# Performance work log

Measured on AMD Instinct MI355X. Metric: run time of the kernel, lower is better.

## Reference

```python
import jax, jax.numpy as jnp
import numpy as np

# parameter limits (low, high) as in Filter_param.limits
LIMITS = {
    'f_start': (200.0, 4000.0),
    'f_inf': (20.0, 500.0),
    'f_decay': (0.0, 2.0),
    'f_T': (0.0, 2.0),
    'w_offset': (0.0, 1.0),
    'w_T': (0.01, 0.5),
}

B, T = 2048, 8192

def setup_inputs() -> dict:
    key = jax.random.key(0)
    ks = jax.random.split(key, 7)
    return {
        'X': jax.random.normal(ks[0], (B, T), dtype=jnp.float32),
        'F': 44100,  # sampling frequency (int constant)
        'f_start_normal': jax.random.normal(ks[1], (), dtype=jnp.float32),
        'f_inf_normal': jax.random.normal(ks[2], (), dtype=jnp.float32),
        'f_decay_normal': jax.random.normal(ks[3], (), dtype=jnp.float32),
        'f_T_normal': jax.random.normal(ks[4], (), dtype=jnp.float32),
        'w_offset_normal': jax.random.normal(ks[5], (), dtype=jnp.float32),
        'w_T_normal': jax.random.normal(ks[6], (), dtype=jnp.float32),
    }

def _squash(v, name):
    low, high = LIMITS[name]
    return low + (high - low) * jax.nn.sigmoid(v)

def reference(X, F, f_start_normal, f_inf_normal, f_decay_normal,
              f_T_normal, w_offset_normal, w_T_normal):
    Bsz, Tlen = X.shape
    c = (2.0 ** (1.0 / 3.0) - 1.0) ** 0.5 * F / np.pi  # scalar cutoff constant
    t = jnp.arange(Tlen, dtype=X.dtype) / Tlen  # normalized time [T]

    f_start = _squash(f_start_normal, 'f_start')
    f_inf = _squash(f_inf_normal, 'f_inf')
    f_decay = _squash(f_decay_normal, 'f_decay')
    f_T = _squash(f_T_normal, 'f_T')
    w_offset = _squash(w_offset_normal, 'w_offset')
    w_T = _squash(w_T_normal, 'w_T')

    # time-varying cutoff frequency and output window
    f = f_inf + (f_start - f_inf) * (0.7 * 0.1 ** f_decay) ** (t / (10.0 * 0.1 ** f_T))  # [T]
    w = jax.nn.sigmoid((t - w_offset) / w_T)  # [T]
    a = (f - c) / (f + c)  # [T]
    b = (a + 1.0) / 2.0    # [T]

    # cascaded time-varying one-pole recurrence (two stages), scanned over time.
    # t=0: y1 = y2 = X[:,0];   t>0:
    #   y1[t] = b[t]*(x[t] + x[t-1]) - a[t]*y1[t-1]
    #   y2[t] = b[t]*(y1[t] + y1[t-1]) - a[t]*y2[t-1]
    x0 = X[:, 0]
    init = (x0, x0, x0, w[0] * x0)  # (y0_prev, y1_prev, y2_prev, acc)

    def step(carry, inp):
        y0p, y1p, y2p, acc = carry
        x_t, a_t, b_t, w_t = inp
        y1 = b_t * (x_t + y0p) - a_t * y1p
        y2 = b_t * (y1 + y1p) - a_t * y2p
        return (x_t, y1, y2, acc + w_t * y2), None

    xs = (X[:, 1:].T, a[1:], b[1:], w[1:])  # time-major [T-1, ...]
    (_, _, _, acc), _ = jax.lax.scan(step, init, xs)

    return acc / jnp.sum(w)  # prediction [B]
```

## Files before the change

### kernel.cpp

```cpp
#include <hip/hip_runtime.h>
#include <math.h>

#define BB 2048
#define TT 8192
#define CC 128
#define LL 64

#define OFF_SC  2048
#define OFF_Q   4096

__device__ inline float sigmoid_dev(float v) { return 1.0f / (1.0f + expf(-v)); }
__device__ inline float squash_dev(float v, float lo, float hi) {
    return lo + (hi - lo) * sigmoid_dev(v);
}

struct SquashedParams {
    float c, f_start, f_inf, log2K_invTd, w_offset, inv_w_T;
};

__device__ inline SquashedParams load_params(const int* Fp,
                                             const float* p_fstart, const float* p_finf,
                                             const float* p_fdecay, const float* p_fT,
                                             const float* p_woff, const float* p_wT) {
    SquashedParams P;
    float Fv      = (float)(*Fp);
    P.c           = sqrtf(exp2f(1.0f / 3.0f) - 1.0f) * Fv / 3.14159265358979323846f;
    P.f_start     = squash_dev(*p_fstart, 200.0f, 4000.0f);
    P.f_inf       = squash_dev(*p_finf,   20.0f,  500.0f);
    float f_decay = squash_dev(*p_fdecay, 0.0f,   2.0f);
    float f_T     = squash_dev(*p_fT,     0.0f,   2.0f);
    P.w_offset    = squash_dev(*p_woff,   0.0f,   1.0f);
    float w_T     = squash_dev(*p_wT,     0.01f,  0.5f);
    P.inv_w_T     = 1.0f / w_T;
    const float LOG2_10 = 3.32192809488736235f;
    float log2K  = log2f(0.7f) - LOG2_10 * f_decay;
    float invTd  = 0.1f * exp2f(LOG2_10 * f_T);
    P.log2K_invTd = log2K * invTd;
    return P;
}

__device__ inline float4 step_coef(const SquashedParams& P, int tg) {
    if (tg >= TT - 1) return make_float4(0.0f, 0.0f, 0.0f, 0.0f);
    float ti = (float)(tg + 1) * (1.0f / (float)TT);
    float f  = P.f_inf + (P.f_start - P.f_inf) * exp2f(P.log2K_invTd * ti);
    float a  = (f - P.c) / (f + P.c);
    float b  = 0.5f * (a + 1.0f);
    float m  = -a;
    float p  = b * (1.0f + m);
    float w  = sigmoid_dev((ti - P.w_offset) * P.inv_w_T);
    return make_float4(m, b, p, w);
}

__global__ void setup_kernel(const int* Fp,
                             const float* p_fstart, const float* p_finf,
                             const float* p_fdecay, const float* p_fT,
                             const float* p_woff, const float* p_wT,
                             float4* __restrict__ A4, float* __restrict__ SC) {
    int j = threadIdx.x;
    SquashedParams P = load_params(Fp, p_fstart, p_finf, p_fdecay, p_fT, p_woff, p_wT);
    float al = 1.0f, be = 0.0f, ga = 0.0f, de = 0.0f, ws = 0.0f;
    for (int k = 0; k < LL; k++) {
        float4 c4 = step_coef(P, j * LL + k);
        float m = c4.x, p = c4.z, w = c4.w;
        float nal = m * al;
        float nbe = fmaf(p, al, m * be);
        de = fmaf(w * m, al, de);
        ga = fmaf(w, nbe, ga);
        al = nal; be = nbe;
        ws += w;
    }
    A4[j] = make_float4(al, be, ga, de);

    __shared__ float sws[CC];
    sws[j] = ws;
    __syncthreads();
    for (int s = CC / 2; s > 0; s >>= 1) {
        if (j < s) sws[j] += sws[j + s];
        __syncthreads();
    }
    if (j == 0) {
        float w0 = sigmoid_dev((0.0f - P.w_offset) * P.inv_w_T);
        float tot = w0 + sws[0];
        SC[0] = 1.0f / tot;
        SC[1] = w0;
    }
}

__global__ void chunk_kernel(const float* __restrict__ X,
                             const int* Fp,
                             const float* p_fstart, const float* p_finf,
                             const float* p_fdecay, const float* p_fT,
                             const float* p_woff, const float* p_wT,
                             float4* __restrict__ Q4) {
    int j = blockIdx.x >> 3;
    int b = ((blockIdx.x & 7) << 8) + threadIdx.x;

    __shared__ float4 sc[LL];
    if (threadIdx.x < LL) {
        SquashedParams P = load_params(Fp, p_fstart, p_finf, p_fdecay, p_fT, p_woff, p_wT);
        sc[threadIdx.x] = step_coef(P, j * LL + threadIdx.x);
    }
    __syncthreads();

    const float* base = X + (size_t)b * TT + j * LL;
    float e[LL];
    #pragma unroll
    for (int i = 0; i < LL / 4; i++) {
        float4 v = reinterpret_cast<const float4*>(base)[i];
        e[4 * i + 0] = v.x; e[4 * i + 1] = v.y;
        e[4 * i + 2] = v.z; e[4 * i + 3] = v.w;
    }
    float e_next = (j < CC - 1) ? base[LL] : 0.0f;

    float y1 = 0.0f, y2 = 0.0f, acc = 0.0f;
    #pragma unroll
    for (int k = 0; k < LL; k++) {
        float4 c4 = sc[k];
        float x  = (k < LL - 1) ? e[k + 1] : e_next;
        float xp = e[k];
        float u  = c4.y * (x + xp);
        float y2n = fmaf(c4.x, y2, fmaf(c4.z, y1, c4.y * u));
        y1 = fmaf(c4.x, y1, u);
        y2 = y2n;
        acc = fmaf(c4.w, y2n, acc);
    }
    Q4[j * BB + b] = make_float4(y1, y2, acc, 0.0f);
}

__global__ void combine_kernel(const float* __restrict__ X,
                               const float4* __restrict__ A4, const float* __restrict__ SC,
                               const float4* __restrict__ Q4, float* __restrict__ out) {
    int wid  = threadIdx.x >> 6;
    int lane = threadIdx.x & 63;
    int r    = (blockIdx.x << 2) + wid;
    int c0   = lane << 1;

    float x0 = X[(size_t)r * TT];
    float4 Aa = A4[c0], Ab = A4[c0 + 1];
    float4 qa = Q4[(size_t)c0 * BB + r];
    float4 qb = Q4[(size_t)(c0 + 1) * BB + r];

    float al = Ab.x * Aa.x;
    float be = fmaf(Ab.y, Aa.x, Ab.x * Aa.y);
    float ga = fmaf(Ab.z, Aa.x, fmaf(Ab.w, Aa.y, Aa.z));
    float de = fmaf(Ab.w, Aa.x, Aa.w);
    float q1 = fmaf(Ab.x, qa.x, qb.x);
    float q2 = fmaf(Ab.y, qa.x, fmaf(Ab.x, qa.y, qb.y));
    float q3 = fmaf(Ab.z, qa.x, fmaf(Ab.w, qa.y, qa.z + qb.z));

    #pragma unroll
    for (int o = 1; o < 64; o <<= 1) {
        float al2 = __shfl_down(al, o);
        float be2 = __shfl_down(be, o);
        float ga2 = __shfl_down(ga, o);
        float de2 = __shfl_down(de, o);
        float q12 = __shfl_down(q1, o);
        float q22 = __shfl_down(q2, o);
        float q32 = __shfl_down(q3, o);
        float nal = al2 * al;
        float nbe = fmaf(be2, al, al2 * be);
        float nga = fmaf(ga2, al, fmaf(de2, be, ga));
        float nde = fmaf(de2, al, de);
        float nq1 = fmaf(al2, q1, q12);
        float nq2 = fmaf(be2, q1, fmaf(al2, q2, q22));
        float nq3 = fmaf(ga2, q1, fmaf(de2, q2, q3 + q32));
        al = nal; be = nbe; ga = nga; de = nde; q1 = nq1; q2 = nq2; q3 = nq3;
    }

    if (lane == 0) {
        float w0 = SC[1];
        float accf = fmaf(ga + de + w0, x0, q3);
        out[r] = accf * SC[0];
    }
}

extern "C" void kernel_launch(void* const* d_in, const int* in_sizes, int n_in,
                              void* d_out, int out_size, void* d_ws, size_t ws_size,
                              hipStream_t stream) {
    const float* X        = (const float*)d_in[0];
    const int*   Fp       = (const int*)d_in[1];
    const float* p_fstart = (const float*)d_in[2];
    const float* p_finf   = (const float*)d_in[3];
    const float* p_fdecay = (const float*)d_in[4];
    const float* p_fT     = (const float*)d_in[5];
    const float* p_woff   = (const float*)d_in[6];
    const float* p_wT     = (const float*)d_in[7];
    float* out = (float*)d_out;

    char* ws = (char*)d_ws;
    float4* A4 = (float4*)ws;
    float*  SC = (float*)(ws + OFF_SC);
    float4* Q4 = (float4*)(ws + OFF_Q);

    setup_kernel<<<1, CC, 0, stream>>>(Fp, p_fstart, p_finf, p_fdecay, p_fT,
                                       p_woff, p_wT, A4, SC);
    chunk_kernel<<<CC * 8, 256, 0, stream>>>(X, Fp, p_fstart, p_finf, p_fdecay,
                                             p_fT, p_woff, p_wT, Q4);
    combine_kernel<<<BB / 4, 256, 0, stream>>>(X, A4, SC, Q4, out);
}
```

Baseline: 124.7 us.

## Fuse setup, chunk scan and combine into one per-row kernel

Replaces the three launches (coefficient setup, per-chunk scan, cross-chunk combine) with one kernel where each block handles two rows and each thread scans one 64-step segment. Each thread computes its own step coefficients and chunk transfer matrices inline, and the result is reduced with warp shuffles plus a small shared-memory merge of two half-row waves. This removes the Q4 workspace round trip and two extra launches, and switches sigmoid to the fast __expf. In exchange every thread redundantly recomputes per-step coefficients (exp2, divides, sigmoid) that were shared before, which raises ALU work per element. The loads also change from batch-strided to row-contiguous per segment.

```diff
diff --git a/kernel.cpp b/kernel.cpp
--- a/kernel.cpp
+++ b/kernel.cpp
@@ -3,13 +3,10 @@
 
 #define BB 2048
 #define TT 8192
-#define CC 128
-#define LL 64
+#define NSEG 128
+#define SL 64
 
-#define OFF_SC  2048
-#define OFF_Q   4096
-
-__device__ inline float sigmoid_dev(float v) { return 1.0f / (1.0f + expf(-v)); }
+__device__ inline float sigmoid_dev(float v) { return 1.0f / (1.0f + __expf(-v)); }
 __device__ inline float squash_dev(float v, float lo, float hi) {
     return lo + (hi - lo) * sigmoid_dev(v);
 }
@@ -39,29 +36,58 @@
     return P;
 }
 
-__device__ inline float4 step_coef(const SquashedParams& P, int tg) {
-    if (tg >= TT - 1) return make_float4(0.0f, 0.0f, 0.0f, 0.0f);
-    float ti = (float)(tg + 1) * (1.0f / (float)TT);
-    float f  = P.f_inf + (P.f_start - P.f_inf) * exp2f(P.log2K_invTd * ti);
-    float a  = (f - P.c) / (f + P.c);
-    float b  = 0.5f * (a + 1.0f);
-    float m  = -a;
-    float p  = b * (1.0f + m);
-    float w  = sigmoid_dev((ti - P.w_offset) * P.inv_w_T);
-    return make_float4(m, b, p, w);
-}
+__global__ __launch_bounds__(256, 4)
+void fused_kernel(const float* __restrict__ X,
+                  const int* Fp,
+                  const float* p_fstart, const float* p_finf,
+                  const float* p_fdecay, const float* p_fT,
+                  const float* p_woff, const float* p_wT,
+                  float* __restrict__ out) {
+    const int tid  = threadIdx.x;
+    const int lane = tid & 63;
+    const int wid  = tid >> 6;
+    const int rloc = wid >> 1;
+    const int half = wid & 1;
+    const int row  = (blockIdx.x << 1) + rloc;
+    const int seg  = (half << 6) + lane;
 
-__global__ void setup_kernel(const int* Fp,
-                             const float* p_fstart, const float* p_finf,
-                             const float* p_fdecay, const float* p_fT,
-                             const float* p_woff, const float* p_wT,
-                             float4* __restrict__ A4, float* __restrict__ SC) {
-    int j = threadIdx.x;
     SquashedParams P = load_params(Fp, p_fstart, p_finf, p_fdecay, p_fT, p_woff, p_wT);
+
+    const float* base = X + (size_t)row * TT + seg * SL;
+    float e[SL];
+    #pragma unroll
+    for (int i = 0; i < SL / 4; i++) {
+        float4 v = reinterpret_cast<const float4*>(base)[i];
+        e[4 * i + 0] = v.x; e[4 * i + 1] = v.y;
+        e[4 * i + 2] = v.z; e[4 * i + 3] = v.w;
+    }
+    float xn = 0.0f;
+    if (seg < NSEG - 1) xn = base[SL];
+
+    const float dti     = 1.0f / (float)TT;
+    const float ti_base = (float)(seg * SL + 1) * dti;
+    const float df      = P.f_start - P.f_inf;
+
+    float y1 = 0.0f, y2 = 0.0f, q3 = 0.0f;
     float al = 1.0f, be = 0.0f, ga = 0.0f, de = 0.0f, ws = 0.0f;
-    for (int k = 0; k < LL; k++) {
-        float4 c4 = step_coef(P, j * LL + k);
-        float m = c4.x, p = c4.z, w = c4.w;
+    #pragma unroll
+    for (int k = 0; k < SL; k++) {
+        float ti = fmaf((float)k, dti, ti_base);
+        float f  = fmaf(df, exp2f(P.log2K_invTd * ti), P.f_inf);
+        float r  = 1.0f / (f + P.c);
+        float b  = f * r;
+        float m  = (P.c - f) * r;
+        float p  = b * (1.0f + m);
+        float w  = sigmoid_dev((ti - P.w_offset) * P.inv_w_T);
+        if (seg == NSEG - 1 && k == SL - 1) { m = 0.0f; b = 0.0f; p = 0.0f; w = 0.0f; }
+
+        float x  = (k < SL - 1) ? e[k + 1] : xn;
+        float u  = b * (x + e[k]);
+        float y2n = fmaf(m, y2, fmaf(p, y1, b * u));
+        y1 = fmaf(m, y1, u);
+        y2 = y2n;
+        q3 = fmaf(w, y2n, q3);
+
         float nal = m * al;
         float nbe = fmaf(p, al, m * be);
         de = fmaf(w * m, al, de);
@@ -69,84 +95,7 @@
         al = nal; be = nbe;
         ws += w;
     }
-    A4[j] = make_float4(al, be, ga, de);
-
-    __shared__ float sws[CC];
-    sws[j] = ws;
-    __syncthreads();
-    for (int s = CC / 2; s > 0; s >>= 1) {
-        if (j < s) sws[j] += sws[j + s];
-        __syncthreads();
-    }
-    if (j == 0) {
-        float w0 = sigmoid_dev((0.0f - P.w_offset) * P.inv_w_T);
-        float tot = w0 + sws[0];
-        SC[0] = 1.0f / tot;
-        SC[1] = w0;
-    }
-}
-
-__global__ void chunk_kernel(const float* __restrict__ X,
-                             const int* Fp,
-                             const float* p_fstart, const float* p_finf,
-                             const float* p_fdecay, const float* p_fT,
-                             const float* p_woff, const float* p_wT,
-                             float4* __restrict__ Q4) {
-    int j = blockIdx.x >> 3;
-    int b = ((blockIdx.x & 7) << 8) + threadIdx.x;
-
-    __shared__ float4 sc[LL];
-    if (threadIdx.x < LL) {
-        SquashedParams P = load_params(Fp, p_fstart, p_finf, p_fdecay, p_fT, p_woff, p_wT);
-        sc[threadIdx.x] = step_coef(P, j * LL + threadIdx.x);
-    }
-    __syncthreads();
-
-    const float* base = X + (size_t)b * TT + j * LL;
-    float e[LL];
-    #pragma unroll
-    for (int i = 0; i < LL / 4; i++) {
-        float4 v = reinterpret_cast<const float4*>(base)[i];
-        e[4 * i + 0] = v.x; e[4 * i + 1] = v.y;
-        e[4 * i + 2] = v.z; e[4 * i + 3] = v.w;
-    }
-    float e_next = (j < CC - 1) ? base[LL] : 0.0f;
-
-    float y1 = 0.0f, y2 = 0.0f, acc = 0.0f;
-    #pragma unroll
-    for (int k = 0; k < LL; k++) {
-        float4 c4 = sc[k];
-        float x  = (k < LL - 1) ? e[k + 1] : e_next;
-        float xp = e[k];
-        float u  = c4.y * (x + xp);
-        float y2n = fmaf(c4.x, y2, fmaf(c4.z, y1, c4.y * u));
-        y1 = fmaf(c4.x, y1, u);
-        y2 = y2n;
-        acc = fmaf(c4.w, y2n, acc);
-    }
-    Q4[j * BB + b] = make_float4(y1, y2, acc, 0.0f);
-}
-
-__global__ void combine_kernel(const float* __restrict__ X,
-                               const float4* __restrict__ A4, const float* __restrict__ SC,
-                               const float4* __restrict__ Q4, float* __restrict__ out) {
-    int wid  = threadIdx.x >> 6;
-    int lane = threadIdx.x & 63;
-    int r    = (blockIdx.x << 2) + wid;
-    int c0   = lane << 1;
-
-    float x0 = X[(size_t)r * TT];
-    float4 Aa = A4[c0], Ab = A4[c0 + 1];
-    float4 qa = Q4[(size_t)c0 * BB + r];
-    float4 qb = Q4[(size_t)(c0 + 1) * BB + r];
-
-    float al = Ab.x * Aa.x;
-    float be = fmaf(Ab.y, Aa.x, Ab.x * Aa.y);
-    float ga = fmaf(Ab.z, Aa.x, fmaf(Ab.w, Aa.y, Aa.z));
-    float de = fmaf(Ab.w, Aa.x, Aa.w);
-    float q1 = fmaf(Ab.x, qa.x, qb.x);
-    float q2 = fmaf(Ab.y, qa.x, fmaf(Ab.x, qa.y, qb.y));
-    float q3 = fmaf(Ab.z, qa.x, fmaf(Ab.w, qa.y, qa.z + qb.z));
+    float q1 = y1, q2 = y2;
 
     #pragma unroll
     for (int o = 1; o < 64; o <<= 1) {
@@ -157,6 +106,7 @@
         float q12 = __shfl_down(q1, o);
         float q22 = __shfl_down(q2, o);
         float q32 = __shfl_down(q3, o);
+        float ws2 = __shfl_down(ws, o);
         float nal = al2 * al;
         float nbe = fmaf(be2, al, al2 * be);
         float nga = fmaf(ga2, al, fmaf(de2, be, ga));
@@ -164,13 +114,34 @@
         float nq1 = fmaf(al2, q1, q12);
         float nq2 = fmaf(be2, q1, fmaf(al2, q2, q22));
         float nq3 = fmaf(ga2, q1, fmaf(de2, q2, q3 + q32));
-        al = nal; be = nbe; ga = nga; de = nde; q1 = nq1; q2 = nq2; q3 = nq3;
+        al = nal; be = nbe; ga = nga; de = nde;
+        q1 = nq1; q2 = nq2; q3 = nq3; ws += ws2;
     }
 
+    __shared__ float sred[4][8];
+    __shared__ float sx0[2];
     if (lane == 0) {
-        float w0 = SC[1];
-        float accf = fmaf(ga + de + w0, x0, q3);
-        out[r] = accf * SC[0];
+        sred[wid][0] = al; sred[wid][1] = be; sred[wid][2] = ga; sred[wid][3] = de;
+        sred[wid][4] = q1; sred[wid][5] = q2; sred[wid][6] = q3; sred[wid][7] = ws;
+        if (half == 0) sx0[rloc] = e[0];
+    }
+    __syncthreads();
+
+    if (tid < 2) {
+        int r = tid;
+        const float* E = sred[2 * r + 0];
+        const float* L = sred[2 * r + 1];
+        float alE = E[0], beE = E[1], gaE = E[2], deE = E[3];
+        float q1E = E[4], q2E = E[5], q3E = E[6];
+        float gaL = L[2], deL = L[3], q3L = L[6];
+        float ga_f = fmaf(gaL, alE, fmaf(deL, beE, gaE));
+        float de_f = fmaf(deL, alE, deE);
+        float q3_f = fmaf(gaL, q1E, fmaf(deL, q2E, q3E + q3L));
+        float x0 = sx0[r];
+        float w0 = sigmoid_dev((0.0f - P.w_offset) * P.inv_w_T);
+        float sumw = E[7] + L[7] + w0;
+        float accf = fmaf(ga_f + de_f + w0, x0, q3_f);
+        out[(blockIdx.x << 1) + r] = accf / sumw;
     }
 }
 
@@ -187,14 +158,6 @@
     const float* p_wT     = (const float*)d_in[7];
     float* out = (float*)d_out;
 
-    char* ws = (char*)d_ws;
-    float4* A4 = (float4*)ws;
-    float*  SC = (float*)(ws + OFF_SC);
-    float4* Q4 = (float4*)(ws + OFF_Q);
-
-    setup_kernel<<<1, CC, 0, stream>>>(Fp, p_fstart, p_finf, p_fdecay, p_fT,
-                                       p_woff, p_wT, A4, SC);
-    chunk_kernel<<<CC * 8, 256, 0, stream>>>(X, Fp, p_fstart, p_finf, p_fdecay,
-                                             p_fT, p_woff, p_wT, Q4);
-    combine_kernel<<<BB / 4, 256, 0, stream>>>(X, A4, SC, Q4, out);
+    fused_kernel<<<BB / 2, 256, 0, stream>>>(X, Fp, p_fstart, p_finf, p_fdecay,
+                                             p_fT, p_woff, p_wT, out);
 }
```

Result: faster. 121.9 us (-2.3%).
